# Kernel optimization log

Hardware: AMD Instinct MI355X
Metric: run time of the kernel (lower is better)

The kernel has to match this reference:

```python
import jax, jax.numpy as jnp
import numpy as np
import math

M = 512          # num_bin_x
NB = 512         # num_bin_y
NUM_NODES = 2_000_000
K = 4            # max bins a node can overlap per dim (size <= 2.5 bins)
SQRT2 = math.sqrt(2.0)


def setup_inputs() -> dict:
    key = jax.random.key(0)
    k1, k2 = jax.random.split(key)
    node_pos = jax.random.uniform(k1, (NUM_NODES, 2), jnp.float32, 0.05, 0.95)
    # node sizes between 0.5 and 2.5 bins (normalized layout units)
    node_size = jax.random.uniform(k2, (NUM_NODES, 2), jnp.float32) * (2.0 / M) + (0.5 / M)
    return {
        "node_pos": node_pos,
        "node_size": node_size,
        "node_weight": jnp.ones((NUM_NODES,), jnp.float32),
        "expand_ratio": jnp.ones((NUM_NODES,), jnp.float32),
        "unit_len": jnp.array([1.0 / M, 1.0 / NB], jnp.float32),
        "init_density_map": jnp.zeros((M, NB), jnp.float32),
        "num_bin_x": M,
        "num_bin_y": NB,
    }


def pre_normalize(node_pos, node_size, node_weight, expand_ratio, unit_len, mx, ny):
    # density_map_cuda.pre_normalize: expand tiny nodes to sqrt(2)*unit_len,
    # rescale weight to preserve area, convert rects to bin coordinates.
    ux, uy = unit_len[0], unit_len[1]
    w, h = node_size[:, 0], node_size[:, 1]
    new_w = jnp.maximum(w, SQRT2 * ux)
    new_h = jnp.maximum(h, SQRT2 * uy)
    weight = node_weight * expand_ratio * (w * h) / (new_w * new_h)
    xl = jnp.clip((node_pos[:, 0] - 0.5 * new_w) / ux, 0.0, mx)
    xh = jnp.clip((node_pos[:, 0] + 0.5 * new_w) / ux, 0.0, mx)
    yl = jnp.clip((node_pos[:, 1] - 0.5 * new_h) / uy, 0.0, ny)
    yh = jnp.clip((node_pos[:, 1] + 0.5 * new_h) / uy, 0.0, ny)
    return jnp.stack([xl, xh, yl, yh, weight], axis=1)  # [N, 5]


def scatter_density(info, mx, ny):
    # density_map_cuda.forward: overlap-area scatter-add of node rects into bins.
    xl, xh, yl, yh, w = info[:, 0], info[:, 1], info[:, 2], info[:, 3], info[:, 4]
    bx0 = jnp.floor(xl).astype(jnp.int32)
    by0 = jnp.floor(yl).astype(jnp.int32)
    dm = jnp.zeros((mx, ny), jnp.float32)
    for dx in range(K):
        ix = bx0 + dx
        fx = ix.astype(jnp.float32)
        ox = jnp.clip(jnp.minimum(xh, fx + 1.0) - jnp.maximum(xl, fx), 0.0)
        ixc = jnp.clip(ix, 0, mx - 1)
        for dy in range(K):
            iy = by0 + dy
            fy = iy.astype(jnp.float32)
            oy = jnp.clip(jnp.minimum(yh, fy + 1.0) - jnp.maximum(yl, fy), 0.0)
            iyc = jnp.clip(iy, 0, ny - 1)
            dm = dm.at[ixc, iyc].add(w * ox * oy)
    return dm


def make_transforms(n):
    k = jnp.arange(n, dtype=jnp.float32)[:, None]
    m = jnp.arange(n, dtype=jnp.float32)[None, :]
    ang = jnp.pi * k * (2.0 * m + 1.0) / (2.0 * n)
    C = jnp.cos(ang)  # [freq, space]
    S = jnp.sin(ang)
    w = jnp.where(jnp.arange(n) == 0, 1.0, 2.0).astype(jnp.float32)
    return C, S, w


def spectral_solve(dm, unit_len, mx, ny):
    # fft_scale construction from __init__
    wj = (jnp.arange(mx, dtype=jnp.float32) * (2.0 * jnp.pi / mx))[:, None]
    wk = (jnp.arange(ny, dtype=jnp.float32) * (2.0 * jnp.pi / ny))[None, :]
    wk = wk * (unit_len[0] / unit_len[1])  # scale_w_k=True
    wsq = wj ** 2 + wk ** 2
    wsq = wsq.at[0, 0].set(1.0)
    pscale = (1.0 / wsq).at[0, 0].set(0.0)
    fx_scale = wj * pscale * 0.5
    fy_scale = wk * pscale * 0.5

    Cx, Sx, wx = make_transforms(mx)
    Cy, Sy, wy = make_transforms(ny)
    # dct2: coeff[u,v] = (1/(M*N)) * sum_{m,n} dm[m,n] cos(pi u(2m+1)/2M) cos(pi v(2n+1)/2N)
    coeff = (Cx @ dm @ Cy.T) / (mx * ny)
    ICx = (wx[:, None] * Cx)  # weighted inverse cosine basis [freq, space]
    ICy = (wy[:, None] * Cy)
    ISx = (wx[:, None] * Sx)
    ISy = (wy[:, None] * Sy)
    potential = ICx.T @ (coeff * pscale) @ ICy          # idct2
    force_x = ISx.T @ (coeff * fx_scale) @ ICy          # idxst_idct
    force_y = ICx.T @ (coeff * fy_scale) @ ISy          # idct_idxst
    return potential, force_x, force_y


def reference(node_pos, node_size, node_weight, expand_ratio, unit_len,
              init_density_map, num_bin_x, num_bin_y):
    info = pre_normalize(node_pos, node_size, node_weight, expand_ratio,
                         unit_len, num_bin_x, num_bin_y)
    density_map = init_density_map + scatter_density(info, num_bin_x, num_bin_y)
    potential, _, _ = spectral_solve(density_map, unit_len, num_bin_x, num_bin_y)
    energy = jnp.sum(potential * density_map)
    return energy
```

## Files before the change

### kernel.cpp

```cpp
#include <hip/hip_runtime.h>
#include <math.h>

#define MX 512
#define NY 512
#define TWO_PI 6.283185307179586f

#define TSHIFT 6
#define NT 64
#define LDIM 68
#define SLAB (LDIM * LDIM)
#define SLAB4 (SLAB / 4)
#define NPB 2048
#define KPT 8
#define CAP 40960
#define SPTMAX 32
#define RPARTS 19
#define QSCALE 26214.0f
#define QINV (1.0f / 26214.0f)

typedef __attribute__((ext_vector_type(8))) short short8;
typedef __attribute__((ext_vector_type(4))) float float4_t;
typedef __attribute__((ext_vector_type(4))) unsigned short ushort4_t;

__device__ __forceinline__ unsigned short f2bf(float x) {
    union { float f; unsigned u; } v; v.f = x;
    unsigned r = v.u + 0x7fffu + ((v.u >> 16) & 1u);
    return (unsigned short)(r >> 16);
}
__device__ __forceinline__ float bf2f(unsigned short h) {
    union { float f; unsigned u; } v; v.u = ((unsigned)h) << 16;
    return v.f;
}

__device__ __forceinline__ void node_bounds(float2 p, float2 s, float ux, float uy,
                                            float& xl, float& xh, float& yl, float& yh,
                                            float& nw, float& nh) {
    const float SQ2 = 1.41421356237309515f;
    nw = fmaxf(s.x, SQ2 * ux);
    nh = fmaxf(s.y, SQ2 * uy);
    xl = fminf(fmaxf((p.x - 0.5f * nw) / ux, 0.0f), (float)MX);
    xh = fminf(fmaxf((p.x + 0.5f * nw) / ux, 0.0f), (float)MX);
    yl = fminf(fmaxf((p.y - 0.5f * nh) / uy, 0.0f), (float)NY);
    yh = fminf(fmaxf((p.y + 0.5f * nh) / uy, 0.0f), (float)NY);
}

__global__ void gen_cos_kernel(unsigned short* __restrict__ Ch,
                               unsigned short* __restrict__ Cl,
                               unsigned int* __restrict__ base,
                               unsigned int* __restrict__ cursor,
                               float* __restrict__ out, int cap_mode) {
    int idx = blockIdx.x * blockDim.x + threadIdx.x;
    if (idx == 0) *out = 0.0f;
    if (cap_mode && idx <= NT) {
        base[idx] = (unsigned int)idx * CAP;
        if (idx < NT) cursor[idx] = (unsigned int)idx * CAP;
    }
    int a = idx >> 9;
    int j = idx & 511;
    float x = cospif((float)(a * (2 * j + 1)) * (1.0f / 1024.0f));
    unsigned short hi = f2bf(x);
    Ch[idx] = hi;
    Cl[idx] = f2bf(x - bf2f(hi));
}

__global__ __launch_bounds__(256)
void count_kernel(const float2* __restrict__ pos, const float2* __restrict__ size,
                  const float* __restrict__ unit_len,
                  unsigned int* __restrict__ cnt, int n) {
    __shared__ unsigned int h[NT];
    if (threadIdx.x < NT) h[threadIdx.x] = 0;
    __syncthreads();
    float ux = unit_len[0], uy = unit_len[1];
    int start = blockIdx.x * NPB;
    int end = min(start + NPB, n);
#pragma unroll
    for (int k = 0; k < KPT; k++) {
        int i = start + k * 256 + (int)threadIdx.x;
        if (i < end) {
            float xl, xh, yl, yh, nw, nh;
            node_bounds(pos[i], size[i], ux, uy, xl, xh, yl, yh, nw, nh);
            int bx0 = min((int)floorf(xl), MX - 1);
            int by0 = min((int)floorf(yl), NY - 1);
            atomicAdd(&h[((bx0 >> TSHIFT) << 3) | (by0 >> TSHIFT)], 1u);
        }
    }
    __syncthreads();
    if (threadIdx.x < NT) {
        unsigned int c = h[threadIdx.x];
        if (c) atomicAdd(&cnt[threadIdx.x], c);
    }
}

__global__ void scan_kernel(const unsigned int* __restrict__ cnt,
                            unsigned int* __restrict__ base,
                            unsigned int* __restrict__ cursor) {
    if (threadIdx.x == 0 && blockIdx.x == 0) {
        unsigned int ex = 0;
        for (int t = 0; t < NT; t++) {
            base[t] = ex;
            cursor[t] = ex;
            ex += cnt[t];
        }
        base[NT] = ex;
    }
}

__global__ __launch_bounds__(256)
void place_kernel(const float2* __restrict__ pos, const float2* __restrict__ size,
                  const float* __restrict__ nwt, const float* __restrict__ er,
                  const float* __restrict__ unit_len,
                  const unsigned int* __restrict__ base,
                  unsigned int* __restrict__ cursor,
                  float4* __restrict__ pb, int n) {
    __shared__ unsigned int h[NT];
    __shared__ unsigned int lb[NT + 1];
    __shared__ unsigned int bb[NT];
    __shared__ float4 buf[NPB];
    __shared__ unsigned char til[NPB];
    if (threadIdx.x < NT) h[threadIdx.x] = 0;
    __syncthreads();
    float ux = unit_len[0], uy = unit_len[1];
    int start = blockIdx.x * NPB;
    int end = min(start + NPB, n);

    float cxl[KPT], cyl[KPT], cw[KPT];
    unsigned int cq[KPT], pk[KPT];
#pragma unroll
    for (int k = 0; k < KPT; k++) {
        int i = start + k * 256 + (int)threadIdx.x;
        if (i < end) {
            float2 p = pos[i], s = size[i];
            float xl, xh, yl, yh, nw, nh;
            node_bounds(p, s, ux, uy, xl, xh, yl, yh, nw, nh);
            cxl[k] = xl; cyl[k] = yl;
            cw[k] = nwt[i] * er[i] * (s.x * s.y) / (nw * nh);
            unsigned qx = (unsigned)((xh - xl) * QSCALE + 0.5f);
            unsigned qy = (unsigned)((yh - yl) * QSCALE + 0.5f);
            if (qx > 65535u) qx = 65535u;
            if (qy > 65535u) qy = 65535u;
            cq[k] = qx | (qy << 16);
            int bx0 = min((int)floorf(xl), MX - 1);
            int by0 = min((int)floorf(yl), NY - 1);
            unsigned int t = ((bx0 >> TSHIFT) << 3) | (by0 >> TSHIFT);
            pk[k] = (t << 11) | atomicAdd(&h[t], 1u);
        }
    }
    __syncthreads();
    if (threadIdx.x == 0) {
        unsigned int ex = 0;
        for (int t = 0; t < NT; t++) { lb[t] = ex; ex += h[t]; }
        lb[NT] = ex;
    }
    if (threadIdx.x < NT) {
        unsigned int c = h[threadIdx.x];
        bb[threadIdx.x] = c ? atomicAdd(&cursor[threadIdx.x], c) : 0u;
    }
    __syncthreads();
#pragma unroll
    for (int k = 0; k < KPT; k++) {
        int i = start + k * 256 + (int)threadIdx.x;
        if (i < end) {
            unsigned int t = pk[k] >> 11;
            unsigned int slot = lb[t] + (pk[k] & 2047u);
            buf[slot] = make_float4(cxl[k], cyl[k], cw[k], __uint_as_float(cq[k]));
            til[slot] = (unsigned char)t;
        }
    }
    __syncthreads();
    unsigned int total = lb[NT];
    for (unsigned int j = threadIdx.x; j < total; j += 256) {
        unsigned int t = til[j];
        unsigned int dst = bb[t] + (j - lb[t]);
        if (dst < base[t + 1]) pb[dst] = buf[j];
    }
}

__device__ __forceinline__ void accum_one(float4 v, float* acc, int tbx, int tby) {
    float xl = v.x, yl = v.y, w = v.z;
    unsigned q = __float_as_uint(v.w);
    float xh = xl + (float)(q & 0xffffu) * QINV;
    float yh = yl + (float)(q >> 16) * QINV;
    int bx0 = min((int)floorf(xl), MX - 1);
    int by0 = min((int)floorf(yl), NY - 1);
    float oxs[4], oys[4];
    int rb[4], lys[4];
#pragma unroll
    for (int d = 0; d < 4; d++) {
        int ix = bx0 + d;
        float fx = (float)ix;
        oxs[d] = fmaxf(fminf(xh, fx + 1.0f) - fmaxf(xl, fx), 0.0f);
        rb[d] = (min(ix, MX - 1) - tbx) * LDIM;
        int iy = by0 + d;
        float fy = (float)iy;
        oys[d] = fmaxf(fminf(yh, fy + 1.0f) - fmaxf(yl, fy), 0.0f);
        lys[d] = min(iy, NY - 1) - tby;
    }
#pragma unroll
    for (int dx = 0; dx < 4; dx++) {
        if (oxs[dx] == 0.0f) continue;
        float wox = w * oxs[dx];
#pragma unroll
        for (int dy = 0; dy < 4; dy++) {
            float vv = wox * oys[dy];
            if (vv != 0.0f) atomicAdd(&acc[rb[dx] + lys[dy]], vv);
        }
    }
}

__global__ __launch_bounds__(256)
void accum_kernel(const float4* __restrict__ pb,
                  const unsigned int* __restrict__ base,
                  const unsigned int* __restrict__ cursor,
                  float* __restrict__ slab, int spt) {
    __shared__ float acc[SLAB];
    int t = blockIdx.x / spt;
    int s = blockIdx.x - t * spt;
    int tbx = (t >> 3) << TSHIFT;
    int tby = (t & 7) << TSHIFT;
    for (int e = threadIdx.x; e < SLAB4; e += 256)
        ((float4*)acc)[e] = make_float4(0.f, 0.f, 0.f, 0.f);
    __syncthreads();

    unsigned int b0 = base[t];
    unsigned int c = min(cursor[t] - b0, base[t + 1] - b0);
    unsigned int chunk = (c + spt - 1) / spt;
    unsigned int ks = s * chunk;
    unsigned int ke = min(c, ks + chunk);

    unsigned int k = ks + threadIdx.x;
    float4 cur = make_float4(0.f, 0.f, 0.f, 0.f);
    bool have = (k < ke);
    if (have) cur = pb[b0 + k];
    while (have) {
        unsigned int k2 = k + 256;
        bool have2 = (k2 < ke);
        float4 nxt = make_float4(0.f, 0.f, 0.f, 0.f);
        if (have2) nxt = pb[b0 + k2];
        accum_one(cur, acc, tbx, tby);
        cur = nxt; k = k2; have = have2;
    }
    __syncthreads();

    float4* dst = (float4*)(slab + (size_t)blockIdx.x * SLAB);
    for (int e = threadIdx.x; e < SLAB4; e += 256)
        dst[e] = ((float4*)acc)[e];
}

__global__ __launch_bounds__(256)
void reduce_slabs_kernel(const float* __restrict__ slab,
                         float* __restrict__ tacc, int spt) {
    int t = blockIdx.x / RPARTS;
    int part = blockIdx.x - t * RPARTS;
    int e = part * 256 + (int)threadIdx.x;
    if (e < SLAB) {
        const float* s0 = slab + (size_t)t * spt * SLAB + e;
        float sum = 0.0f;
        for (int s = 0; s < spt; s++) sum += s0[(size_t)s * SLAB];
        tacc[(size_t)t * SLAB + e] = sum;
    }
}

__global__ __launch_bounds__(256)
void combine_kernel(const float* __restrict__ tacc,
                    const float* __restrict__ init_dm,
                    unsigned short* __restrict__ dmh,
                    unsigned short* __restrict__ dml) {
    int v = blockIdx.x * blockDim.x + threadIdx.x;
    int gx = v >> 7;
    int g4 = v & 127;
    int gy = g4 << 2;
    int rx = gx & 63, ry = gy & 63;
    int tx0 = gx >> TSHIFT, ty0 = gy >> TSHIFT;

    float4 sum = ((const float4*)init_dm)[v];
#pragma unroll
    for (int ax = 0; ax < 2; ax++) {
        int tx = tx0 - ax;
        if (tx < 0 || (ax == 1 && rx > 3)) continue;
        int lx = rx + (ax << TSHIFT);
#pragma unroll
        for (int ay = 0; ay < 2; ay++) {
            int ty = ty0 - ay;
            if (ty < 0 || (ay == 1 && ry > 0)) continue;
            int ly = ry + (ay << TSHIFT);
            float4 sv = *(const float4*)(tacc
                + (size_t)((tx << 3) | ty) * SLAB + lx * LDIM + ly);
            sum.x += sv.x; sum.y += sv.y; sum.z += sv.z; sum.w += sv.w;
        }
    }
    ushort4_t hi, lo;
    float sv[4] = {sum.x, sum.y, sum.z, sum.w};
#pragma unroll
    for (int r = 0; r < 4; r++) {
        unsigned short h = f2bf(sv[r]);
        hi[r] = h;
        lo[r] = f2bf(sv[r] - bf2f(h));
    }
    int idx = (gx << 9) | gy;
    *(ushort4_t*)(dmh + idx) = hi;
    *(ushort4_t*)(dml + idx) = lo;
}

__global__ __launch_bounds__(256)
void scatter_kernel(const float2* __restrict__ pos, const float2* __restrict__ size,
                    const float* __restrict__ nwt, const float* __restrict__ er,
                    const float* __restrict__ unit_len,
                    float* __restrict__ dm, int n) {
    int i = blockIdx.x * blockDim.x + threadIdx.x;
    if (i >= n) return;
    float ux = unit_len[0], uy = unit_len[1];
    float2 p = pos[i], s = size[i];
    float xl, xh, yl, yh, nw, nh;
    node_bounds(p, s, ux, uy, xl, xh, yl, yh, nw, nh);
    float w = nwt[i] * er[i] * (s.x * s.y) / (nw * nh);
    int bx0 = (int)floorf(xl);
    int by0 = (int)floorf(yl);
#pragma unroll
    for (int dx = 0; dx < 4; dx++) {
        int ix = bx0 + dx;
        float fx = (float)ix;
        float ox = fmaxf(fminf(xh, fx + 1.0f) - fmaxf(xl, fx), 0.0f);
        if (ox == 0.0f) continue;
        int rowoff = min(max(ix, 0), MX - 1) * NY;
        float wox = w * ox;
#pragma unroll
        for (int dy = 0; dy < 4; dy++) {
            int iy = by0 + dy;
            float fy = (float)iy;
            float oy = fmaxf(fminf(yh, fy + 1.0f) - fmaxf(yl, fy), 0.0f);
            float vv = wox * oy;
            if (vv != 0.0f) atomicAdd(&dm[rowoff + min(max(iy, 0), NY - 1)], vv);
        }
    }
}

__global__ void cvt_dm_kernel(const float* __restrict__ dm,
                              unsigned short* __restrict__ dmh,
                              unsigned short* __restrict__ dml) {
    int idx = blockIdx.x * blockDim.x + threadIdx.x;
    float x = dm[idx];
    unsigned short hi = f2bf(x);
    dmh[idx] = hi;
    dml[idx] = f2bf(x - bf2f(hi));
}

__global__ __launch_bounds__(256)
void dct1_mfma_kernel(const unsigned short* __restrict__ dmh,
                      const unsigned short* __restrict__ dml,
                      const unsigned short* __restrict__ Ch,
                      const unsigned short* __restrict__ Cl,
                      unsigned short* __restrict__ UhT,
                      unsigned short* __restrict__ UlT) {
    int lane = threadIdx.x & 63;
    int wv = threadIdx.x >> 6;
    int tile = blockIdx.x * 4 + wv;
    int jt = (tile >> 5) * 16;
    int bt = (tile & 31) * 16;
    int m = lane & 15, q = lane >> 4;
    float4_t acc = {0.f, 0.f, 0.f, 0.f};
    const unsigned short* ah_row = dmh + (jt + m) * 512;
    const unsigned short* al_row = dml + (jt + m) * 512;
    const unsigned short* bh_row = Ch + (bt + m) * 512;
    const unsigned short* bl_row = Cl + (bt + m) * 512;
#pragma unroll 4
    for (int k0 = 0; k0 < 512; k0 += 32) {
        int off = k0 + q * 8;
        short8 ah = *(const short8*)(ah_row + off);
        short8 al = *(const short8*)(al_row + off);
        short8 bh = *(const short8*)(bh_row + off);
        short8 bl = *(const short8*)(bl_row + off);
        acc = __builtin_amdgcn_mfma_f32_16x16x32_bf16(ah, bh, acc, 0, 0, 0);
        acc = __builtin_amdgcn_mfma_f32_16x16x32_bf16(ah, bl, acc, 0, 0, 0);
        acc = __builtin_amdgcn_mfma_f32_16x16x32_bf16(al, bh, acc, 0, 0, 0);
    }
#pragma unroll
    for (int r = 0; r < 4; r++) {
        float v = acc[r];
        unsigned short hi = f2bf(v);
        int addr = (bt + m) * 512 + jt + q * 4 + r;
        UhT[addr] = hi;
        UlT[addr] = f2bf(v - bf2f(hi));
    }
}

__global__ __launch_bounds__(256)
void dct2_mfma_kernel(const unsigned short* __restrict__ Ch,
                      const unsigned short* __restrict__ Cl,
                      const unsigned short* __restrict__ UhT,
                      const unsigned short* __restrict__ UlT,
                      const float* __restrict__ unit_len,
                      float* __restrict__ out) {
    __shared__ float red[4];
    int lane = threadIdx.x & 63;
    int wv = threadIdx.x >> 6;
    int tile = blockIdx.x * 4 + wv;
    int at = (tile >> 5) * 16;
    int bt = (tile & 31) * 16;
    int m = lane & 15, q = lane >> 4;
    float4_t acc = {0.f, 0.f, 0.f, 0.f};
    const unsigned short* ah_row = Ch + (at + m) * 512;
    const unsigned short* al_row = Cl + (at + m) * 512;
    const unsigned short* bh_row = UhT + (bt + m) * 512;
    const unsigned short* bl_row = UlT + (bt + m) * 512;
#pragma unroll 4
    for (int k0 = 0; k0 < 512; k0 += 32) {
        int off = k0 + q * 8;
        short8 ah = *(const short8*)(ah_row + off);
        short8 al = *(const short8*)(al_row + off);
        short8 bh = *(const short8*)(bh_row + off);
        short8 bl = *(const short8*)(bl_row + off);
        acc = __builtin_amdgcn_mfma_f32_16x16x32_bf16(ah, bh, acc, 0, 0, 0);
        acc = __builtin_amdgcn_mfma_f32_16x16x32_bf16(ah, bl, acc, 0, 0, 0);
        acc = __builtin_amdgcn_mfma_f32_16x16x32_bf16(al, bh, acc, 0, 0, 0);
    }
    float ratio = unit_len[0] / unit_len[1];
    int b = bt + m;
    float wkb = (float)b * (TWO_PI / (float)NY) * ratio;
    float wyb = (b == 0) ? 1.0f : 2.0f;
    float e = 0.0f;
#pragma unroll
    for (int r = 0; r < 4; r++) {
        int a = at + q * 4 + r;
        float wja = (float)a * (TWO_PI / (float)MX);
        float wsq = wja * wja + wkb * wkb;
        float ps = (a == 0 && b == 0) ? 0.0f : (1.0f / wsq);
        float wxa = (a == 0) ? 1.0f : 2.0f;
        e += wxa * wyb * ps * acc[r] * acc[r];
    }
#pragma unroll
    for (int off = 32; off > 0; off >>= 1) e += __shfl_down(e, off, 64);
    if (lane == 0) red[wv] = e;
    __syncthreads();
    if (threadIdx.x == 0) {
        float t = red[0] + red[1] + red[2] + red[3];
        atomicAdd(out, t * (1.0f / ((float)MX * (float)NY)));
    }
}

extern "C" void kernel_launch(void* const* d_in, const int* in_sizes, int n_in,
                              void* d_out, int out_size, void* d_ws, size_t ws_size,
                              hipStream_t stream) {
    const float2* node_pos  = (const float2*)d_in[0];
    const float2* node_size = (const float2*)d_in[1];
    const float*  node_wt   = (const float*)d_in[2];
    const float*  exp_ratio = (const float*)d_in[3];
    const float*  unit_len  = (const float*)d_in[4];
    const float*  init_dm   = (const float*)d_in[5];
    float* out = (float*)d_out;
    int n = in_sizes[2];

    char* wsb = (char*)d_ws;
    size_t off = 0;
    auto alloc = [&](size_t bytes) { void* p = wsb + off; off = (off + bytes + 255) & ~(size_t)255; return p; };
    unsigned short* Ch   = (unsigned short*)alloc((size_t)MX * NY * 2);
    unsigned short* Cl   = (unsigned short*)alloc((size_t)MX * NY * 2);
    unsigned short* dmh  = (unsigned short*)alloc((size_t)MX * NY * 2);
    unsigned short* dml  = (unsigned short*)alloc((size_t)MX * NY * 2);
    unsigned short* UhT  = (unsigned short*)alloc((size_t)MX * NY * 2);
    unsigned short* UlT  = (unsigned short*)alloc((size_t)MX * NY * 2);
    float*          dm     = (float*)alloc((size_t)MX * NY * sizeof(float));
    unsigned int*   cnt    = (unsigned int*)alloc(NT * sizeof(unsigned int));
    unsigned int*   tbase  = (unsigned int*)alloc((NT + 1) * sizeof(unsigned int));
    unsigned int*   cursor = (unsigned int*)alloc(NT * sizeof(unsigned int));
    float*          tacc   = (float*)alloc((size_t)NT * SLAB * sizeof(float));
    size_t off_common = off;
    size_t per_spt = (size_t)NT * SLAB * sizeof(float);

    float4* pbF = (float4*)alloc((size_t)NT * CAP * sizeof(float4));
    int sptF = 0;
    float* slbF = nullptr;
    if (off <= ws_size) {
        sptF = (int)((ws_size - off) / per_spt);
        if (sptF > SPTMAX) sptF = SPTMAX;
        if (sptF >= 4) slbF = (float*)alloc((size_t)NT * sptF * SLAB * sizeof(float));
    }
    bool tierFast = (slbF != nullptr);

    off = off_common;
    float4* pbE = (float4*)alloc((size_t)n * sizeof(float4));
    int sptE = 0;
    float* slbE = nullptr;
    if (off <= ws_size) {
        sptE = (int)((ws_size - off) / per_spt);
        if (sptE > SPTMAX) sptE = SPTMAX;
        if (sptE >= 1) slbE = (float*)alloc((size_t)NT * sptE * SLAB * sizeof(float));
    }
    bool tierExact = (slbE != nullptr);

    gen_cos_kernel<<<(MX * NY) / 256, 256, 0, stream>>>(Ch, Cl, tbase, cursor,
                                                        out, tierFast ? 1 : 0);

    if (tierFast || tierExact) {
        float4* pb  = tierFast ? pbF : pbE;
        float*  slb = tierFast ? slbF : slbE;
        int     spt = tierFast ? sptF : sptE;
        int nblk = (n + NPB - 1) / NPB;
        if (!tierFast) {
            hipMemsetAsync(cnt, 0, NT * sizeof(unsigned int), stream);
            count_kernel<<<nblk, 256, 0, stream>>>(node_pos, node_size, unit_len, cnt, n);
            scan_kernel<<<1, 64, 0, stream>>>(cnt, tbase, cursor);
        }
        place_kernel<<<nblk, 256, 0, stream>>>(
            node_pos, node_size, node_wt, exp_ratio, unit_len, tbase, cursor, pb, n);
        accum_kernel<<<NT * spt, 256, 0, stream>>>(pb, tbase, cursor, slb, spt);
        reduce_slabs_kernel<<<NT * RPARTS, 256, 0, stream>>>(slb, tacc, spt);
        combine_kernel<<<256, 256, 0, stream>>>(tacc, init_dm, dmh, dml);
    } else {
        hipMemcpyAsync(dm, init_dm, (size_t)MX * NY * sizeof(float),
                       hipMemcpyDeviceToDevice, stream);
        scatter_kernel<<<(n + 255) / 256, 256, 0, stream>>>(
            node_pos, node_size, node_wt, exp_ratio, unit_len, dm, n);
        cvt_dm_kernel<<<(MX * NY) / 256, 256, 0, stream>>>(dm, dmh, dml);
    }

    dct1_mfma_kernel<<<256, 256, 0, stream>>>(dmh, dml, Ch, Cl, UhT, UlT);
    dct2_mfma_kernel<<<256, 256, 0, stream>>>(Ch, Cl, UhT, UlT, unit_len, out);
}
```

Measured before the change: 239.7 us.

## Split accumulation blocks across tiles in proportion to tile item count

Instead of giving every one of the 64 tiles a fixed number of slab blocks, the accumulate kernel computes per-tile item counts with a wave-level prefix scan and assigns each tile a share of a total block budget proportional to its load. The slab reduction recomputes the same mapping to find each tile's slab range. This is meant to balance work across blocks when tile populations are uneven and to let the block count grow up to the available workspace. In exchange, every block of both kernels redoes the scan over the 64 tiles, and the larger total slab count adds more slab write and read traffic.

```diff
diff --git a/kernel.cpp b/kernel.cpp
--- a/kernel.cpp
+++ b/kernel.cpp
@@ -13,7 +13,6 @@
 #define NPB 2048
 #define KPT 8
 #define CAP 40960
-#define SPTMAX 32
 #define RPARTS 19
 #define QSCALE 26214.0f
 #define QINV (1.0f / 26214.0f)
@@ -211,23 +210,55 @@
 void accum_kernel(const float4* __restrict__ pb,
                   const unsigned int* __restrict__ base,
                   const unsigned int* __restrict__ cursor,
-                  float* __restrict__ slab, int spt) {
+                  float* __restrict__ slab, int T) {
     __shared__ float acc[SLAB];
-    int t = blockIdx.x / spt;
-    int s = blockIdx.x - t * spt;
+    __shared__ int sh_t, sh_done;
+    __shared__ unsigned int sh_ks, sh_ke, sh_b0;
+    int tid = threadIdx.x;
+    if (tid < 64) {
+        unsigned int t = tid;
+        unsigned int b0 = base[t];
+        unsigned int cap = base[t + 1] - b0;
+        unsigned int cr = cursor[t] - b0;
+        unsigned int c = cr < cap ? cr : cap;
+        unsigned int S = c;
+#pragma unroll
+        for (int d = 1; d < 64; d <<= 1) {
+            unsigned int v = __shfl_up(S, d, 64);
+            if (tid >= d) S += v;
+        }
+        unsigned int total = __shfl(S, 63, 64);
+        unsigned int nb = total ? (unsigned int)(((unsigned long long)c * (unsigned int)T) / total) + 1u : 1u;
+        unsigned int Pn = nb;
+#pragma unroll
+        for (int d = 1; d < 64; d <<= 1) {
+            unsigned int v = __shfl_up(Pn, d, 64);
+            if (tid >= d) Pn += v;
+        }
+        unsigned int NBU = __shfl(Pn, 63, 64);
+        unsigned int Pex = Pn - nb;
+        unsigned int b = blockIdx.x;
+        if (tid == 0) sh_done = (b >= NBU) ? 1 : 0;
+        if (b >= Pex && b < Pn) {
+            unsigned int s = b - Pex;
+            unsigned int chunk = nb ? (c + nb - 1) / nb : 0u;
+            unsigned int ks = s * chunk;
+            unsigned int ke = min(c, ks + chunk);
+            sh_t = (int)t; sh_ks = ks; sh_ke = ke; sh_b0 = b0;
+        }
+    }
+    for (int e = tid; e < SLAB4; e += 256)
+        ((float4*)acc)[e] = make_float4(0.f, 0.f, 0.f, 0.f);
+    __syncthreads();
+    if (sh_done) return;
+
+    int t = sh_t;
     int tbx = (t >> 3) << TSHIFT;
     int tby = (t & 7) << TSHIFT;
-    for (int e = threadIdx.x; e < SLAB4; e += 256)
-        ((float4*)acc)[e] = make_float4(0.f, 0.f, 0.f, 0.f);
-    __syncthreads();
-
-    unsigned int b0 = base[t];
-    unsigned int c = min(cursor[t] - b0, base[t + 1] - b0);
-    unsigned int chunk = (c + spt - 1) / spt;
-    unsigned int ks = s * chunk;
-    unsigned int ke = min(c, ks + chunk);
-
-    unsigned int k = ks + threadIdx.x;
+    unsigned int b0 = sh_b0;
+    unsigned int ke = sh_ke;
+
+    unsigned int k = sh_ks + (unsigned int)tid;
     float4 cur = make_float4(0.f, 0.f, 0.f, 0.f);
     bool have = (k < ke);
     if (have) cur = pb[b0 + k];
@@ -242,20 +273,48 @@
     __syncthreads();
 
     float4* dst = (float4*)(slab + (size_t)blockIdx.x * SLAB);
-    for (int e = threadIdx.x; e < SLAB4; e += 256)
+    for (int e = tid; e < SLAB4; e += 256)
         dst[e] = ((float4*)acc)[e];
 }
 
 __global__ __launch_bounds__(256)
 void reduce_slabs_kernel(const float* __restrict__ slab,
-                         float* __restrict__ tacc, int spt) {
+                         float* __restrict__ tacc,
+                         const unsigned int* __restrict__ base,
+                         const unsigned int* __restrict__ cursor, int T) {
+    __shared__ unsigned int sh_P, sh_nb;
     int t = blockIdx.x / RPARTS;
     int part = blockIdx.x - t * RPARTS;
-    int e = part * 256 + (int)threadIdx.x;
+    int tid = threadIdx.x;
+    if (tid < 64) {
+        unsigned int tt = tid;
+        unsigned int b0 = base[tt];
+        unsigned int cap = base[tt + 1] - b0;
+        unsigned int cr = cursor[tt] - b0;
+        unsigned int c = cr < cap ? cr : cap;
+        unsigned int S = c;
+#pragma unroll
+        for (int d = 1; d < 64; d <<= 1) {
+            unsigned int v = __shfl_up(S, d, 64);
+            if (tid >= d) S += v;
+        }
+        unsigned int total = __shfl(S, 63, 64);
+        unsigned int nb = total ? (unsigned int)(((unsigned long long)c * (unsigned int)T) / total) + 1u : 1u;
+        unsigned int Pn = nb;
+#pragma unroll
+        for (int d = 1; d < 64; d <<= 1) {
+            unsigned int v = __shfl_up(Pn, d, 64);
+            if (tid >= d) Pn += v;
+        }
+        if ((int)tt == t) { sh_P = Pn - nb; sh_nb = nb; }
+    }
+    __syncthreads();
+    int e = part * 256 + tid;
     if (e < SLAB) {
-        const float* s0 = slab + (size_t)t * spt * SLAB + e;
+        const float* s0 = slab + (size_t)sh_P * SLAB + e;
         float sum = 0.0f;
-        for (int s = 0; s < spt; s++) sum += s0[(size_t)s * SLAB];
+        unsigned int nb = sh_nb;
+        for (unsigned int s = 0; s < nb; s++) sum += s0[(size_t)s * SLAB];
         tacc[(size_t)t * SLAB + e] = sum;
     }
 }
@@ -464,26 +523,32 @@
     unsigned int*   cursor = (unsigned int*)alloc(NT * sizeof(unsigned int));
     float*          tacc   = (float*)alloc((size_t)NT * SLAB * sizeof(float));
     size_t off_common = off;
-    size_t per_spt = (size_t)NT * SLAB * sizeof(float);
+    size_t slab_bytes = (size_t)SLAB * sizeof(float);
 
     float4* pbF = (float4*)alloc((size_t)NT * CAP * sizeof(float4));
-    int sptF = 0;
+    int TF = 0;
     float* slbF = nullptr;
     if (off <= ws_size) {
-        sptF = (int)((ws_size - off) / per_spt);
-        if (sptF > SPTMAX) sptF = SPTMAX;
-        if (sptF >= 4) slbF = (float*)alloc((size_t)NT * sptF * SLAB * sizeof(float));
+        size_t navail = (ws_size - off) / slab_bytes;
+        if (navail >= 320) {
+            size_t t = navail - 64;
+            TF = (int)(t > 1984 ? 1984 : t);
+            slbF = (float*)alloc((size_t)(TF + 64) * slab_bytes);
+        }
     }
     bool tierFast = (slbF != nullptr);
 
     off = off_common;
     float4* pbE = (float4*)alloc((size_t)n * sizeof(float4));
-    int sptE = 0;
+    int TE = 0;
     float* slbE = nullptr;
     if (off <= ws_size) {
-        sptE = (int)((ws_size - off) / per_spt);
-        if (sptE > SPTMAX) sptE = SPTMAX;
-        if (sptE >= 1) slbE = (float*)alloc((size_t)NT * sptE * SLAB * sizeof(float));
+        size_t navail = (ws_size - off) / slab_bytes;
+        if (navail >= 128) {
+            size_t t = navail - 64;
+            TE = (int)(t > 1984 ? 1984 : t);
+            slbE = (float*)alloc((size_t)(TE + 64) * slab_bytes);
+        }
     }
     bool tierExact = (slbE != nullptr);
 
@@ -493,7 +558,7 @@
     if (tierFast || tierExact) {
         float4* pb  = tierFast ? pbF : pbE;
         float*  slb = tierFast ? slbF : slbE;
-        int     spt = tierFast ? sptF : sptE;
+        int     T   = tierFast ? TF : TE;
         int nblk = (n + NPB - 1) / NPB;
         if (!tierFast) {
             hipMemsetAsync(cnt, 0, NT * sizeof(unsigned int), stream);
@@ -502,8 +567,8 @@
         }
         place_kernel<<<nblk, 256, 0, stream>>>(
             node_pos, node_size, node_wt, exp_ratio, unit_len, tbase, cursor, pb, n);
-        accum_kernel<<<NT * spt, 256, 0, stream>>>(pb, tbase, cursor, slb, spt);
-        reduce_slabs_kernel<<<NT * RPARTS, 256, 0, stream>>>(slb, tacc, spt);
+        accum_kernel<<<T + 64, 256, 0, stream>>>(pb, tbase, cursor, slb, T);
+        reduce_slabs_kernel<<<NT * RPARTS, 256, 0, stream>>>(slb, tacc, tbase, cursor, T);
         combine_kernel<<<256, 256, 0, stream>>>(tacc, init_dm, dmh, dml);
     } else {
         hipMemcpyAsync(dm, init_dm, (size_t)MX * NY * sizeof(float),
```

Result: no change. 239.1 us (-0.2%).
